# Optimization experiments

Measured on AMD Instinct MI355X. Metric: run time of the kernel, lower is better.

The kernel has to match this reference:

```python
import jax, jax.numpy as jnp
import numpy as np

SIGMA2 = 1.9 * 1.9   # LJ sigma^2 (Angstrom^2)
EPS = 0.2            # LJ well depth
R2_SOFT = 0.25       # softening to keep energies finite for random dofs


def _local_ht(dofs):
    """dofs [..., 9] -> local homogeneous transform [..., 4, 4].
    Uses (phi, theta, d) bond-style dofs: R = Rz(phi) @ Ry(theta),
    translation d along the rotated x-axis."""
    phi, theta = dofs[..., 0], dofs[..., 1]
    d = 1.5 + 0.25 * jnp.tanh(dofs[..., 2])  # bond length ~1.25..1.75 A
    cp, sp = jnp.cos(phi), jnp.sin(phi)
    ct, st = jnp.cos(theta), jnp.sin(theta)
    r00, r01, r02 = cp * ct, -sp, cp * st
    r10, r11, r12 = sp * ct, cp, sp * st
    r20, r21, r22 = -st, jnp.zeros_like(ct), ct
    tx, ty, tz = d * r00, d * r10, d * r20
    zero, one = jnp.zeros_like(phi), jnp.ones_like(phi)
    ht = jnp.stack([
        jnp.stack([r00, r01, r02, tx], -1),
        jnp.stack([r10, r11, r12, ty], -1),
        jnp.stack([r20, r21, r22, tz], -1),
        jnp.stack([zero, zero, zero, one], -1),
    ], -2)
    return ht


def _forward_kin(full_dofs, P, A):
    # per-pose chain kinforest: cumulative left-product of local HTs
    ht = _local_ht(full_dofs.reshape(P, A, 9))  # [P, A, 4, 4]
    compose = lambda a, b: jnp.einsum('...ij,...jk->...ik', a, b)
    cum = jax.lax.associative_scan(compose, ht, axis=1)
    return cum[..., :3, 3].reshape(-1, 3)  # [P*A, 3]


def _lj_score(coords):
    # coords [P, A, 3] -> per-pose softened LJ energy [P]
    sq = jnp.sum(coords * coords, axis=-1)                 # [P, A]
    G = jnp.einsum('pad,pbd->pab', coords, coords)         # [P, A, A] GEMM
    r2 = sq[:, :, None] + sq[:, None, :] - 2.0 * G + R2_SOFT
    inv6 = (SIGMA2 / r2) ** 3
    e = 4.0 * EPS * (inv6 * inv6 - inv6)
    A = coords.shape[1]
    mask = jnp.triu(jnp.ones((A, A), dtype=coords.dtype), k=1)  # i < j
    return jnp.sum(e * mask, axis=(1, 2))


def setup_inputs() -> dict:
    key = jax.random.key(0)
    k1, k2 = jax.random.split(key)
    P, A = 4, 4096
    full_dofs = 0.5 * jax.random.normal(k1, (P * A, 9), dtype=jnp.float32)
    pose_stack_coords = 5.0 * jax.random.normal(k2, (P, A, 3), dtype=jnp.float32)
    kinforest_id = jnp.arange(P * A, dtype=jnp.int64)
    return {"full_dofs": full_dofs, "pose_stack_coords": pose_stack_coords,
            "kinforest_id": kinforest_id}


def reference(full_dofs, pose_stack_coords, kinforest_id):
    P, A, _ = pose_stack_coords.shape
    kincoords = _forward_kin(full_dofs, P, A)  # [P*A, 3]
    coords = pose_stack_coords.reshape(-1, 3).at[kinforest_id].set(kincoords)
    coords = coords.reshape(P, A, 3)
    return _lj_score(coords)  # [P]
```

## Files before the change

### kernel.cpp

```cpp
#include <hip/hip_runtime.h>
#include <math.h>

#define A_ATOMS 4096
#define P_POSES 4
#define N_TOT   (A_ATOMS * P_POSES)
#define TILE    128
#define NTILES  (A_ATOMS / TILE)
#define JG      4
#define NJG     (NTILES / JG)
#define NSTRIPS 144

#define SEG     64
#define NSEG    (A_ATOMS / SEG)
#define APPLY_T 256
#define APPLY_B (A_ATOMS / APPLY_T)

typedef float v2f __attribute__((ext_vector_type(2)));

__device__ __constant__ float c_SIGMA2  = 1.9f * 1.9f;
__device__ __constant__ float c_4EPS    = 0.8f;
__device__ __constant__ float c_R2SOFT  = 0.25f;

struct RT { float m[12]; };

__device__ inline RT rt_identity() {
    RT v;
    v.m[0]=1.f; v.m[1]=0.f; v.m[2]=0.f;  v.m[3]=0.f;
    v.m[4]=0.f; v.m[5]=1.f; v.m[6]=0.f;  v.m[7]=0.f;
    v.m[8]=0.f; v.m[9]=0.f; v.m[10]=1.f; v.m[11]=0.f;
    return v;
}

__device__ inline RT rt_compose(const RT& a, const RT& b) {
    RT c;
#pragma unroll
    for (int i = 0; i < 3; ++i) {
        float a0 = a.m[i*4+0], a1 = a.m[i*4+1], a2 = a.m[i*4+2];
        c.m[i*4+0] = fmaf(a0, b.m[0], fmaf(a1, b.m[4],  a2*b.m[8]));
        c.m[i*4+1] = fmaf(a0, b.m[1], fmaf(a1, b.m[5],  a2*b.m[9]));
        c.m[i*4+2] = fmaf(a0, b.m[2], fmaf(a1, b.m[6],  a2*b.m[10]));
        c.m[i*4+3] = fmaf(a0, b.m[3], fmaf(a1, b.m[7],  fmaf(a2, b.m[11], a.m[i*4+3])));
    }
    return c;
}

__device__ inline RT rt_shfl_up(const RT& a, int off) {
    RT r;
#pragma unroll
    for (int i = 0; i < 12; ++i) r.m[i] = __shfl_up(a.m[i], off, 64);
    return r;
}

__device__ inline RT local_ht(const float* __restrict__ dof) {
    float phi = dof[0], th = dof[1];
    float d = fmaf(0.25f, tanhf(dof[2]), 1.5f);
    float sp, cp, st, ct;
    sincosf(phi, &sp, &cp);
    sincosf(th,  &st, &ct);
    RT h;
    h.m[0] = cp*ct; h.m[1] = -sp; h.m[2]  = cp*st; h.m[3]  = d*cp*ct;
    h.m[4] = sp*ct; h.m[5] =  cp; h.m[6]  = sp*st; h.m[7]  = d*sp*ct;
    h.m[8] = -st;   h.m[9] = 0.f; h.m[10] = ct;    h.m[11] = -d*st;
    return h;
}

__global__ __launch_bounds__(SEG) void fk_scan(const float* __restrict__ dofs,
                                               float* __restrict__ Tx,
                                               float* __restrict__ Ty,
                                               float* __restrict__ Tz,
                                               float4* __restrict__ S0,
                                               float4* __restrict__ S1,
                                               float4* __restrict__ S2) {
    const int pose = blockIdx.x >> 6;
    const int seg  = blockIdx.x & (NSEG - 1);
    const int lane = threadIdx.x;
    const int g    = pose * A_ATOMS + seg * SEG + lane;

    RT v = local_ht(dofs + (size_t)g * 9);

#pragma unroll
    for (int off = 1; off < 64; off <<= 1) {
        RT l = rt_shfl_up(v, off);
        if (lane >= off) v = rt_compose(l, v);
    }

    Tx[g] = v.m[3]; Ty[g] = v.m[7]; Tz[g] = v.m[11];

    if (lane == 63) {
        int s = pose * NSEG + seg;
        S0[s] = make_float4(v.m[0], v.m[1], v.m[2],  v.m[3]);
        S1[s] = make_float4(v.m[4], v.m[5], v.m[6],  v.m[7]);
        S2[s] = make_float4(v.m[8], v.m[9], v.m[10], v.m[11]);
    }
}

__global__ __launch_bounds__(APPLY_T) void fk_apply(const int* __restrict__ kid,
                                                    const float* __restrict__ Tx,
                                                    const float* __restrict__ Ty,
                                                    const float* __restrict__ Tz,
                                                    const float4* __restrict__ S0,
                                                    const float4* __restrict__ S1,
                                                    const float4* __restrict__ S2,
                                                    float* __restrict__ X,
                                                    float* __restrict__ Y,
                                                    float* __restrict__ Z,
                                                    float* __restrict__ out) {
    __shared__ float4 e0[NSEG], e1[NSEG], e2[NSEG];

    const int pose = blockIdx.y;
    const int blk  = blockIdx.x;
    const int tid  = threadIdx.x;
    if (blk == 0 && tid == 0) out[pose] = 0.f;

    if (tid < 64) {
        int s = pose * NSEG + tid;
        float4 a0 = S0[s], a1 = S1[s], a2 = S2[s];
        RT v;
        v.m[0]=a0.x; v.m[1]=a0.y; v.m[2]=a0.z;  v.m[3]=a0.w;
        v.m[4]=a1.x; v.m[5]=a1.y; v.m[6]=a1.z;  v.m[7]=a1.w;
        v.m[8]=a2.x; v.m[9]=a2.y; v.m[10]=a2.z; v.m[11]=a2.w;
#pragma unroll
        for (int off = 1; off < 64; off <<= 1) {
            RT l = rt_shfl_up(v, off);
            if (tid >= off) v = rt_compose(l, v);
        }
        RT ex = rt_shfl_up(v, 1);
        if (tid == 0) ex = rt_identity();
        e0[tid] = make_float4(ex.m[0], ex.m[1], ex.m[2],  ex.m[3]);
        e1[tid] = make_float4(ex.m[4], ex.m[5], ex.m[6],  ex.m[7]);
        e2[tid] = make_float4(ex.m[8], ex.m[9], ex.m[10], ex.m[11]);
    }
    __syncthreads();

    const int a = blk * APPLY_T + tid;
    const int g = pose * A_ATOMS + a;
    float rx = Tx[g], ry = Ty[g], rz = Tz[g];
    float4 x0 = e0[a >> 6], x1 = e1[a >> 6], x2 = e2[a >> 6];
    float tx = fmaf(x0.x, rx, fmaf(x0.y, ry, fmaf(x0.z, rz, x0.w)));
    float ty = fmaf(x1.x, rx, fmaf(x1.y, ry, fmaf(x1.z, rz, x1.w)));
    float tz = fmaf(x2.x, rx, fmaf(x2.y, ry, fmaf(x2.z, rz, x2.w)));
    int dst = kid[g];
    X[dst] = tx; Y[dst] = ty; Z[dst] = tz;
}

__global__ __launch_bounds__(256) void lj_kernel(const float* __restrict__ X,
                                                 const float* __restrict__ Y,
                                                 const float* __restrict__ Z,
                                                 float* __restrict__ out) {
    const int pose = blockIdx.y;
    int rr = blockIdx.x, bi = 0;
    while (rr >= NJG - (bi >> 2)) { rr -= NJG - (bi >> 2); ++bi; }
    const int jg = (bi >> 2) + rr;
    const int t0 = (jg == (bi >> 2)) ? (bi & 3) : 0;

    __shared__ float sxi[TILE], syi[TILE], szi[TILE];
    __shared__ float sxj[TILE], syj[TILE], szj[TILE];

    const int tid = threadIdx.x;
    const float* Xp = X + pose * A_ATOMS;
    const float* Yp = Y + pose * A_ATOMS;
    const float* Zp = Z + pose * A_ATOMS;

    if (tid < TILE) {
        int gi = bi * TILE + tid;
        sxi[tid] = Xp[gi]; syi[tid] = Yp[gi]; szi[tid] = Zp[gi];
    } else {
        int t = tid - TILE;
        int gj = (jg * JG + t0) * TILE + t;
        sxj[t] = Xp[gj]; syj[t] = Yp[gj]; szj[t] = Zp[gj];
    }
    __syncthreads();

    const int i0 = (tid & 15) * 8;
    const int j0 = (tid >> 4) * 8;

    const float SIG2 = c_SIGMA2, SOFT = c_R2SOFT;

    float xi[8], yi[8], zi[8];
#pragma unroll
    for (int k = 0; k < 8; ++k) {
        xi[k] = sxi[i0 + k]; yi[k] = syi[i0 + k]; zi[k] = szi[i0 + k];
    }

    float acc = 0.f;

    for (int t = t0; t < JG; ++t) {
        const int bj = jg * JG + t;

        float px, py, pz;
        if (t < JG - 1 && tid >= TILE) {
            int gj = (bj + 1) * TILE + (tid - TILE);
            px = Xp[gj]; py = Yp[gj]; pz = Zp[gj];
        }

        if (bi != bj) {
            v2f xj2[4], yj2[4], zj2[4];
#pragma unroll
            for (int p = 0; p < 4; ++p) {
                xj2[p] = (v2f){sxj[j0 + 2*p], sxj[j0 + 2*p + 1]};
                yj2[p] = (v2f){syj[j0 + 2*p], syj[j0 + 2*p + 1]};
                zj2[p] = (v2f){szj[j0 + 2*p], szj[j0 + 2*p + 1]};
            }
            const v2f soft2 = (v2f){SOFT, SOFT};
            v2f acc2 = (v2f){0.f, 0.f};
#pragma unroll
            for (int p = 0; p < 4; ++p) {
#pragma unroll
                for (int k = 0; k < 8; ++k) {
                    v2f dx = xi[k] - xj2[p];
                    v2f dy = yi[k] - yj2[p];
                    v2f dz = zi[k] - zj2[p];
                    v2f r2 = __builtin_elementwise_fma(dx, dx,
                             __builtin_elementwise_fma(dy, dy,
                             __builtin_elementwise_fma(dz, dz, soft2)));
                    v2f rc = (v2f){__builtin_amdgcn_rcpf(r2.x), __builtin_amdgcn_rcpf(r2.y)};
                    v2f tt = SIG2 * rc;
                    v2f i6 = tt * tt * tt;
                    acc2 += __builtin_elementwise_fma(i6, i6, -i6);
                }
            }
            acc += acc2.x + acc2.y;
        } else {
            float xj[8], yj[8], zj[8];
#pragma unroll
            for (int k = 0; k < 8; ++k) {
                xj[k] = sxj[j0 + k]; yj[k] = syj[j0 + k]; zj[k] = szj[j0 + k];
            }
#pragma unroll
            for (int jj = 0; jj < 8; ++jj) {
                int j = j0 + jj;
#pragma unroll
                for (int k = 0; k < 8; ++k) {
                    float dx = xi[k] - xj[jj], dy = yi[k] - yj[jj], dz = zi[k] - zj[jj];
                    float r2 = fmaf(dx, dx, fmaf(dy, dy, fmaf(dz, dz, SOFT)));
                    float tt = SIG2 * __builtin_amdgcn_rcpf(r2);
                    float i6 = tt * tt * tt;
                    float hh = fmaf(i6, i6, -i6);
                    acc += ((i0 + k) < j) ? hh : 0.f;
                }
            }
        }

        if (t < JG - 1) {
            __syncthreads();
            if (tid >= TILE) {
                int tl = tid - TILE;
                sxj[tl] = px; syj[tl] = py; szj[tl] = pz;
            }
            __syncthreads();
        }
    }
    acc *= c_4EPS;

#pragma unroll
    for (int off = 32; off > 0; off >>= 1) acc += __shfl_down(acc, off, 64);

    __shared__ float wsum[4];
    int lane = tid & 63, wid = tid >> 6;
    if (lane == 0) wsum[wid] = acc;
    __syncthreads();
    if (tid == 0) {
        float s = wsum[0] + wsum[1] + wsum[2] + wsum[3];
        atomicAdd(out + pose, s);
    }
}

extern "C" void kernel_launch(void* const* d_in, const int* in_sizes, int n_in,
                              void* d_out, int out_size, void* d_ws, size_t ws_size,
                              hipStream_t stream) {
    (void)in_sizes; (void)n_in; (void)out_size; (void)ws_size;
    const float* dofs = (const float*)d_in[0];
    const int*   kid  = (const int*)d_in[2];
    float*       out  = (float*)d_out;

    float* X  = (float*)d_ws;
    float* Y  = X + N_TOT;
    float* Z  = Y + N_TOT;
    float* Tx = Z + N_TOT;
    float* Ty = Tx + N_TOT;
    float* Tz = Ty + N_TOT;
    float4* S0 = (float4*)(Tz + N_TOT);
    float4* S1 = S0 + P_POSES * NSEG;
    float4* S2 = S1 + P_POSES * NSEG;

    fk_scan<<<P_POSES * NSEG, SEG, 0, stream>>>(dofs, Tx, Ty, Tz, S0, S1, S2);
    dim3 agrid(APPLY_B, P_POSES);
    fk_apply<<<agrid, APPLY_T, 0, stream>>>(kid, Tx, Ty, Tz, S0, S1, S2, X, Y, Z, out);
    dim3 grid(NSTRIPS, P_POSES);
    lj_kernel<<<grid, 256, 0, stream>>>(X, Y, Z, out);
}
```

Baseline: 76.84 us.

## Widen LJ j-groups, use 512-thread blocks, float4 coords, double-buffered j tiles

Coordinates are now stored as packed float4 instead of separate X/Y/Z arrays. The LJ kernel moves to 512 threads, each handling 4x8 pairs per tile. j-groups double from 4 to 8 tiles, which cuts the grid to 80 strips per pose, and the j tile is double-buffered so each step needs one barrier instead of two. The aim is fewer redundant i-tile loads, fewer barriers and more latency hiding per block. The cost is fewer blocks (320 total), which may leave the GPU's many CUs underfilled, and 4 bytes of padding per atom in the coordinate array.

```diff
diff --git a/kernel.cpp b/kernel.cpp
--- a/kernel.cpp
+++ b/kernel.cpp
@@ -6,9 +6,10 @@
 #define N_TOT   (A_ATOMS * P_POSES)
 #define TILE    128
 #define NTILES  (A_ATOMS / TILE)
-#define JG      4
+#define JG      8
 #define NJG     (NTILES / JG)
-#define NSTRIPS 144
+#define NSTRIPS 80
+#define LJ_T    512
 
 #define SEG     64
 #define NSEG    (A_ATOMS / SEG)
@@ -101,9 +102,7 @@
                                                     const float4* __restrict__ S0,
                                                     const float4* __restrict__ S1,
                                                     const float4* __restrict__ S2,
-                                                    float* __restrict__ X,
-                                                    float* __restrict__ Y,
-                                                    float* __restrict__ Z,
+                                                    float4* __restrict__ C4,
                                                     float* __restrict__ out) {
     __shared__ float4 e0[NSEG], e1[NSEG], e2[NSEG];
 
@@ -139,74 +138,68 @@
     float tx = fmaf(x0.x, rx, fmaf(x0.y, ry, fmaf(x0.z, rz, x0.w)));
     float ty = fmaf(x1.x, rx, fmaf(x1.y, ry, fmaf(x1.z, rz, x1.w)));
     float tz = fmaf(x2.x, rx, fmaf(x2.y, ry, fmaf(x2.z, rz, x2.w)));
-    int dst = kid[g];
-    X[dst] = tx; Y[dst] = ty; Z[dst] = tz;
-}
-
-__global__ __launch_bounds__(256) void lj_kernel(const float* __restrict__ X,
-                                                 const float* __restrict__ Y,
-                                                 const float* __restrict__ Z,
-                                                 float* __restrict__ out) {
+    C4[kid[g]] = make_float4(tx, ty, tz, 0.f);
+}
+
+__global__ __launch_bounds__(LJ_T) void lj_kernel(const float4* __restrict__ C4,
+                                                  float* __restrict__ out) {
     const int pose = blockIdx.y;
     int rr = blockIdx.x, bi = 0;
-    while (rr >= NJG - (bi >> 2)) { rr -= NJG - (bi >> 2); ++bi; }
-    const int jg = (bi >> 2) + rr;
-    const int t0 = (jg == (bi >> 2)) ? (bi & 3) : 0;
+    while (rr >= NJG - (bi >> 3)) { rr -= NJG - (bi >> 3); ++bi; }
+    const int jg = (bi >> 3) + rr;
+    const int t0 = (jg == (bi >> 3)) ? (bi & 7) : 0;
 
     __shared__ float sxi[TILE], syi[TILE], szi[TILE];
-    __shared__ float sxj[TILE], syj[TILE], szj[TILE];
+    __shared__ float sxj[2][TILE], syj[2][TILE], szj[2][TILE];
 
     const int tid = threadIdx.x;
-    const float* Xp = X + pose * A_ATOMS;
-    const float* Yp = Y + pose * A_ATOMS;
-    const float* Zp = Z + pose * A_ATOMS;
+    const float4* Cp = C4 + pose * A_ATOMS;
 
     if (tid < TILE) {
-        int gi = bi * TILE + tid;
-        sxi[tid] = Xp[gi]; syi[tid] = Yp[gi]; szi[tid] = Zp[gi];
-    } else {
+        float4 c = Cp[bi * TILE + tid];
+        sxi[tid] = c.x; syi[tid] = c.y; szi[tid] = c.z;
+    } else if (tid < 2 * TILE) {
         int t = tid - TILE;
-        int gj = (jg * JG + t0) * TILE + t;
-        sxj[t] = Xp[gj]; syj[t] = Yp[gj]; szj[t] = Zp[gj];
+        float4 c = Cp[(jg * JG + t0) * TILE + t];
+        sxj[0][t] = c.x; syj[0][t] = c.y; szj[0][t] = c.z;
     }
     __syncthreads();
 
-    const int i0 = (tid & 15) * 8;
-    const int j0 = (tid >> 4) * 8;
+    const int i0 = (tid & 31) * 4;
+    const int j0 = (tid >> 5) * 8;
 
     const float SIG2 = c_SIGMA2, SOFT = c_R2SOFT;
 
-    float xi[8], yi[8], zi[8];
-#pragma unroll
-    for (int k = 0; k < 8; ++k) {
+    float xi[4], yi[4], zi[4];
+#pragma unroll
+    for (int k = 0; k < 4; ++k) {
         xi[k] = sxi[i0 + k]; yi[k] = syi[i0 + k]; zi[k] = szi[i0 + k];
     }
 
     float acc = 0.f;
+    int cur = 0;
 
     for (int t = t0; t < JG; ++t) {
         const int bj = jg * JG + t;
 
-        float px, py, pz;
-        if (t < JG - 1 && tid >= TILE) {
-            int gj = (bj + 1) * TILE + (tid - TILE);
-            px = Xp[gj]; py = Yp[gj]; pz = Zp[gj];
-        }
+        float4 p4;
+        const bool pf = (t < JG - 1) && (tid >= 3 * TILE);
+        if (pf) p4 = Cp[(bj + 1) * TILE + (tid - 3 * TILE)];
 
         if (bi != bj) {
             v2f xj2[4], yj2[4], zj2[4];
 #pragma unroll
             for (int p = 0; p < 4; ++p) {
-                xj2[p] = (v2f){sxj[j0 + 2*p], sxj[j0 + 2*p + 1]};
-                yj2[p] = (v2f){syj[j0 + 2*p], syj[j0 + 2*p + 1]};
-                zj2[p] = (v2f){szj[j0 + 2*p], szj[j0 + 2*p + 1]};
+                xj2[p] = (v2f){sxj[cur][j0 + 2*p], sxj[cur][j0 + 2*p + 1]};
+                yj2[p] = (v2f){syj[cur][j0 + 2*p], syj[cur][j0 + 2*p + 1]};
+                zj2[p] = (v2f){szj[cur][j0 + 2*p], szj[cur][j0 + 2*p + 1]};
             }
             const v2f soft2 = (v2f){SOFT, SOFT};
             v2f acc2 = (v2f){0.f, 0.f};
 #pragma unroll
             for (int p = 0; p < 4; ++p) {
 #pragma unroll
-                for (int k = 0; k < 8; ++k) {
+                for (int k = 0; k < 4; ++k) {
                     v2f dx = xi[k] - xj2[p];
                     v2f dy = yi[k] - yj2[p];
                     v2f dz = zi[k] - zj2[p];
@@ -224,13 +217,13 @@
             float xj[8], yj[8], zj[8];
 #pragma unroll
             for (int k = 0; k < 8; ++k) {
-                xj[k] = sxj[j0 + k]; yj[k] = syj[j0 + k]; zj[k] = szj[j0 + k];
+                xj[k] = sxj[cur][j0 + k]; yj[k] = syj[cur][j0 + k]; zj[k] = szj[cur][j0 + k];
             }
 #pragma unroll
             for (int jj = 0; jj < 8; ++jj) {
                 int j = j0 + jj;
 #pragma unroll
-                for (int k = 0; k < 8; ++k) {
+                for (int k = 0; k < 4; ++k) {
                     float dx = xi[k] - xj[jj], dy = yi[k] - yj[jj], dz = zi[k] - zj[jj];
                     float r2 = fmaf(dx, dx, fmaf(dy, dy, fmaf(dz, dz, SOFT)));
                     float tt = SIG2 * __builtin_amdgcn_rcpf(r2);
@@ -242,12 +235,12 @@
         }
 
         if (t < JG - 1) {
+            if (pf) {
+                int tl = tid - 3 * TILE;
+                sxj[1 - cur][tl] = p4.x; syj[1 - cur][tl] = p4.y; szj[1 - cur][tl] = p4.z;
+            }
             __syncthreads();
-            if (tid >= TILE) {
-                int tl = tid - TILE;
-                sxj[tl] = px; syj[tl] = py; szj[tl] = pz;
-            }
-            __syncthreads();
+            cur ^= 1;
         }
     }
     acc *= c_4EPS;
@@ -255,12 +248,14 @@
 #pragma unroll
     for (int off = 32; off > 0; off >>= 1) acc += __shfl_down(acc, off, 64);
 
-    __shared__ float wsum[4];
+    __shared__ float wsum[LJ_T / 64];
     int lane = tid & 63, wid = tid >> 6;
     if (lane == 0) wsum[wid] = acc;
     __syncthreads();
     if (tid == 0) {
-        float s = wsum[0] + wsum[1] + wsum[2] + wsum[3];
+        float s = 0.f;
+#pragma unroll
+        for (int w = 0; w < LJ_T / 64; ++w) s += wsum[w];
         atomicAdd(out + pose, s);
     }
 }
@@ -273,19 +268,17 @@
     const int*   kid  = (const int*)d_in[2];
     float*       out  = (float*)d_out;
 
-    float* X  = (float*)d_ws;
-    float* Y  = X + N_TOT;
-    float* Z  = Y + N_TOT;
-    float* Tx = Z + N_TOT;
-    float* Ty = Tx + N_TOT;
-    float* Tz = Ty + N_TOT;
+    float4* C4 = (float4*)d_ws;
+    float*  Tx = (float*)(C4 + N_TOT);
+    float*  Ty = Tx + N_TOT;
+    float*  Tz = Ty + N_TOT;
     float4* S0 = (float4*)(Tz + N_TOT);
     float4* S1 = S0 + P_POSES * NSEG;
     float4* S2 = S1 + P_POSES * NSEG;
 
     fk_scan<<<P_POSES * NSEG, SEG, 0, stream>>>(dofs, Tx, Ty, Tz, S0, S1, S2);
     dim3 agrid(APPLY_B, P_POSES);
-    fk_apply<<<agrid, APPLY_T, 0, stream>>>(kid, Tx, Ty, Tz, S0, S1, S2, X, Y, Z, out);
+    fk_apply<<<agrid, APPLY_T, 0, stream>>>(kid, Tx, Ty, Tz, S0, S1, S2, C4, out);
     dim3 grid(NSTRIPS, P_POSES);
-    lj_kernel<<<grid, 256, 0, stream>>>(X, Y, Z, out);
-}
+    lj_kernel<<<grid, LJ_T, 0, stream>>>(C4, out);
+}
```

After: 79.77 us. 1.04x slower.
